# Kernel optimization log

Hardware: AMD Instinct MI355X
Metric: run time of the kernel (lower is better)

## Reference

```python
import jax, jax.numpy as jnp
import numpy as np

TOP_K = 8
N_GROUP = 8
TOPK_GROUP = 4
ROUTED_SCALING = 2.5
NORM_TOPK_PROB = True


def setup_inputs() -> dict:
    key = jax.random.key(0)
    k1, k2, k3 = jax.random.split(key, 3)
    bsz, seq_len, h = 4, 4096, 4096
    n_experts = 256
    hidden_states = jax.random.normal(k1, (bsz, seq_len, h), dtype=jnp.float32)
    # kaiming_uniform_(a=sqrt(5)) -> uniform(-1/sqrt(h), 1/sqrt(h)) approximately
    bound = 1.0 / np.sqrt(h)
    weight = jax.random.uniform(k2, (n_experts, h), dtype=jnp.float32, minval=-bound, maxval=bound)
    # correction bias is a buffer, zero-init; give it small random values to exercise the path
    e_score_correction_bias = jax.random.normal(k3, (n_experts,), dtype=jnp.float32) * 0.01
    return {"hidden_states": hidden_states, "weight": weight,
            "e_score_correction_bias": e_score_correction_bias}


def reference(hidden_states, weight, e_score_correction_bias):
    bsz, seq_len, h = hidden_states.shape
    n_experts = weight.shape[0]
    x = hidden_states.reshape(-1, h).astype(jnp.float32)          # [N, h]
    logits = jnp.einsum('nh,eh->ne', x, weight.astype(jnp.float32))  # [N, E]
    scores = jax.nn.sigmoid(logits)                                # [N, E]
    scores_for_choice = scores + e_score_correction_bias[None, :]  # [N, E]

    # group-limited routing: score each group by sum of its top-2 expert scores
    grouped = scores_for_choice.reshape(-1, N_GROUP, n_experts // N_GROUP)
    group_scores = jax.lax.top_k(grouped, 2)[0].sum(axis=-1)       # [N, G]
    _, group_idx = jax.lax.top_k(group_scores, TOPK_GROUP)         # [N, Kg]
    group_mask = jax.nn.one_hot(group_idx, N_GROUP, dtype=scores.dtype).sum(axis=1)  # [N, G]
    score_mask = jnp.repeat(group_mask, n_experts // N_GROUP, axis=-1)               # [N, E]

    tmp_scores = jnp.where(score_mask > 0, scores_for_choice, 0.0)
    _, topk_idx = jax.lax.top_k(tmp_scores, TOP_K)                 # [N, K]
    topk_weight = jnp.take_along_axis(scores, topk_idx, axis=1)    # [N, K] (no bias)

    if TOP_K > 1 and NORM_TOPK_PROB:
        denom = topk_weight.sum(axis=-1, keepdims=True) + 1e-20
        topk_weight = topk_weight / denom
    topk_weight = topk_weight * ROUTED_SCALING
    return topk_idx, topk_weight
```

## Files before the change

### kernel.cpp

```cpp
#include <hip/hip_runtime.h>
#include <math.h>

#define NTOK 16384
#define H 4096
#define NE 256
#define EPS_E 1.2e-5f
#define EPS_G 2.4e-5f
#define FIXCAP 1024
#define FLAGCAP 8192

typedef __attribute__((ext_vector_type(8))) short short8;
typedef __attribute__((ext_vector_type(4))) float f32x4;

__device__ __forceinline__ unsigned short f2bf(float x) {
    union { float f; unsigned u; } v; v.f = x;
    unsigned r = v.u + 0x7FFF + ((v.u >> 16) & 1);
    return (unsigned short)(r >> 16);
}
__device__ __forceinline__ float bf2f(unsigned short h) {
    union { float f; unsigned u; } v; v.u = ((unsigned)h) << 16;
    return v.f;
}

__global__ __launch_bounds__(256)
void split_w(const float* __restrict__ W, unsigned short* __restrict__ whi,
             unsigned short* __restrict__ wlo, int* __restrict__ ws)
{
    if (blockIdx.x == 0 && threadIdx.x == 0) ws[0] = 0;
    const int i = (blockIdx.x * 256 + threadIdx.x) * 4;
    float4 w4 = *(const float4*)(W + i);
    const float wv[4] = {w4.x, w4.y, w4.z, w4.w};
    ushort4 hh, ll;
    unsigned short* hp = (unsigned short*)&hh;
    unsigned short* lp = (unsigned short*)&ll;
    #pragma unroll
    for (int j = 0; j < 4; ++j) {
        unsigned short h = f2bf(wv[j]);
        hp[j] = h;
        lp[j] = f2bf(wv[j] - bf2f(h));
    }
    *(ushort4*)(whi + i) = hh;
    *(ushort4*)(wlo + i) = ll;
}

__global__ __launch_bounds__(256, 3)
void gemm3(const float* __restrict__ X, const unsigned short* __restrict__ Whi,
           const unsigned short* __restrict__ Wlo, float* __restrict__ logits,
           int m_base)
{
    __shared__ __align__(16) unsigned short smem[24576];
    unsigned short* Ah = smem;
    unsigned short* Al = smem + 4096;
    unsigned short* Bh = smem + 8192;
    unsigned short* Bl = smem + 16384;

    const int t = threadIdx.x;
    const int lane = t & 63;
    const int w = t >> 6;
    const int wm = w >> 1, wn = w & 1;
    const int fr = lane & 15, fq = lane >> 4;

    const int G = (int)gridDim.x;
    const int swz = (blockIdx.x & 7) * (G >> 3) + (blockIdx.x >> 3);
    const int nb = swz & 1;
    const int mb = swz >> 1;
    const int mloc = mb * 64;
    const int m0 = m_base + mloc;
    const int e0 = nb * 128;

    f32x4 acc[2][4];
    #pragma unroll
    for (int a = 0; a < 2; ++a)
        #pragma unroll
        for (int b = 0; b < 4; ++b) acc[a][b] = (f32x4){0.f, 0.f, 0.f, 0.f};

    const int ar = t >> 2;
    const int akc = t & 3;
    const float* gxa = X + (size_t)(m0 + ar) * H + akc * 16;

    const int blr = lane >> 3;
    const int bsrc = (lane & 7) ^ blr;
    const unsigned short* gbh = Whi + (size_t)(e0 + w * 8 + blr) * H + bsrc * 8;
    const unsigned short* gbl = Wlo + (size_t)(e0 + w * 8 + blr) * H + bsrc * 8;

    float4 xr0, xr1, xr2, xr3;
    auto loadX = [&](int kt) {
        const float* p = gxa + (size_t)kt * 64;
        xr0 = *(const float4*)p;       xr1 = *(const float4*)(p + 4);
        xr2 = *(const float4*)(p + 8); xr3 = *(const float4*)(p + 12);
    };

    loadX(0);

    #pragma unroll 1
    for (int kt = 0; kt < 64; ++kt) {
        __builtin_amdgcn_sched_barrier(0);
        __builtin_amdgcn_s_barrier();
        __builtin_amdgcn_sched_barrier(0);
        const size_t k0 = (size_t)kt * 64;
        #pragma unroll
        for (int i = 0; i < 4; ++i) {
            __builtin_amdgcn_global_load_lds(
                (const __attribute__((address_space(1))) void*)(gbh + (size_t)(32 * i) * H + k0),
                (__attribute__((address_space(3))) void*)&Bh[(w * 8 + 32 * i) * 64], 16, 0, 0);
            __builtin_amdgcn_global_load_lds(
                (const __attribute__((address_space(1))) void*)(gbl + (size_t)(32 * i) * H + k0),
                (__attribute__((address_space(3))) void*)&Bl[(w * 8 + 32 * i) * 64], 16, 0, 0);
        }
        __builtin_amdgcn_sched_barrier(0);
        asm volatile("s_waitcnt vmcnt(8)" ::: "memory");
        __builtin_amdgcn_sched_barrier(0);
        {
            const float xf[16] = {xr0.x, xr0.y, xr0.z, xr0.w, xr1.x, xr1.y, xr1.z, xr1.w,
                                  xr2.x, xr2.y, xr2.z, xr2.w, xr3.x, xr3.y, xr3.z, xr3.w};
            short8 h0, h1, l0, l1;
            #pragma unroll
            for (int j = 0; j < 16; ++j) {
                union { float f; unsigned u; } uu; uu.f = xf[j];
                union { unsigned u; float f; } hh; hh.u = uu.u & 0xFFFF0000u;
                union { float f; unsigned u; } ll; ll.f = xf[j] - hh.f;
                unsigned short hs = (unsigned short)(uu.u >> 16);
                unsigned short ls = (unsigned short)(ll.u >> 16);
                if (j < 8) { h0[j] = (short)hs; l0[j] = (short)ls; }
                else       { h1[j - 8] = (short)hs; l1[j - 8] = (short)ls; }
            }
            const int c0 = akc * 2;
            const int p0 = (c0 ^ (ar & 7)) * 8, p1 = ((c0 + 1) ^ (ar & 7)) * 8;
            *(short8*)&Ah[ar * 64 + p0] = h0;
            *(short8*)&Ah[ar * 64 + p1] = h1;
            *(short8*)&Al[ar * 64 + p0] = l0;
            *(short8*)&Al[ar * 64 + p1] = l1;
        }
        loadX(kt + 1 < 64 ? kt + 1 : 63);
        __builtin_amdgcn_sched_barrier(0);
        asm volatile("s_waitcnt vmcnt(4) lgkmcnt(0)" ::: "memory");
        __builtin_amdgcn_sched_barrier(0);
        __builtin_amdgcn_s_barrier();
        __builtin_amdgcn_sched_barrier(0);
        #pragma unroll
        for (int kk = 0; kk < 2; ++kk) {
            short8 ah[2], al[2], bh[4], bl[4];
            #pragma unroll
            for (int mt = 0; mt < 2; ++mt) {
                const int r = wm * 32 + mt * 16 + fr;
                const int pos = ((kk * 4 + fq) ^ (r & 7)) * 8;
                ah[mt] = *(const short8*)&Ah[r * 64 + pos];
                al[mt] = *(const short8*)&Al[r * 64 + pos];
            }
            #pragma unroll
            for (int nt = 0; nt < 4; ++nt) {
                const int r = wn * 64 + nt * 16 + fr;
                const int pos = ((kk * 4 + fq) ^ (r & 7)) * 8;
                bh[nt] = *(const short8*)&Bh[r * 64 + pos];
                bl[nt] = *(const short8*)&Bl[r * 64 + pos];
            }
            #pragma unroll
            for (int mt = 0; mt < 2; ++mt)
                #pragma unroll
                for (int nt = 0; nt < 4; ++nt)
                    acc[mt][nt] = __builtin_amdgcn_mfma_f32_16x16x32_bf16(ah[mt], bh[nt], acc[mt][nt], 0, 0, 0);
            #pragma unroll
            for (int mt = 0; mt < 2; ++mt)
                #pragma unroll
                for (int nt = 0; nt < 4; ++nt)
                    acc[mt][nt] = __builtin_amdgcn_mfma_f32_16x16x32_bf16(ah[mt], bl[nt], acc[mt][nt], 0, 0, 0);
            #pragma unroll
            for (int mt = 0; mt < 2; ++mt)
                #pragma unroll
                for (int nt = 0; nt < 4; ++nt)
                    acc[mt][nt] = __builtin_amdgcn_mfma_f32_16x16x32_bf16(al[mt], bh[nt], acc[mt][nt], 0, 0, 0);
        }
    }
    asm volatile("" :: "v"(xr0.x), "v"(xr1.x), "v"(xr2.x), "v"(xr3.x));

    #pragma unroll
    for (int mt = 0; mt < 2; ++mt)
        #pragma unroll
        for (int nt = 0; nt < 4; ++nt)
            #pragma unroll
            for (int r = 0; r < 4; ++r)
                logits[(size_t)(mloc + wm * 32 + mt * 16 + fq * 4 + r) * NE +
                       (e0 + wn * 64 + nt * 16 + fr)] = acc[mt][nt][r];
}

__global__ __launch_bounds__(256)
void route(const float* __restrict__ logits, const float* __restrict__ bias,
           float* __restrict__ out, int* __restrict__ ws, int cap, int m_base)
{
    const int t = threadIdx.x, lane = t & 63, wv = t >> 6;
    const float4 bf4 = *(const float4*)(bias + lane * 4);
    const float bfa[4] = {bf4.x, bf4.y, bf4.z, bf4.w};

    #pragma unroll 1
    for (int tt = 0; tt < 8; ++tt) {
        const int local = blockIdx.x * 32 + wv * 8 + tt;
        const int n = m_base + local;
        const float4 lg = *(const float4*)&logits[(size_t)local * NE + lane * 4];
        const float lga[4] = {lg.x, lg.y, lg.z, lg.w};
        float s[4], sc[4];
        #pragma unroll
        for (int i = 0; i < 4; ++i) {
            s[i] = 1.f / (1.f + expf(-lga[i]));
            sc[i] = s[i] + bfa[i];
        }
        float a1 = fmaxf(sc[0], sc[1]), a2 = fminf(sc[0], sc[1]);
        float b1 = fmaxf(sc[2], sc[3]), b2 = fminf(sc[2], sc[3]);
        float t1 = fmaxf(a1, b1);
        float t2 = fmaxf(fminf(a1, b1), fmaxf(a2, b2));
        #pragma unroll
        for (int off = 1; off <= 4; off <<= 1) {
            float o1 = __shfl_xor(t1, off, 64);
            float o2 = __shfl_xor(t2, off, 64);
            float n1 = fmaxf(t1, o1);
            float n2 = fmaxf(fminf(t1, o1), fmaxf(t2, o2));
            t1 = n1; t2 = n2;
        }
        const float gsum = t1 + t2;
        float gsv[8];
        #pragma unroll
        for (int g = 0; g < 8; ++g) gsv[g] = __shfl(gsum, g * 8, 64);

        float minsel = 3e38f, maxuns = -3e38f;
        bool sel = false;
        const int myg = lane >> 3;
        #pragma unroll
        for (int g = 0; g < 8; ++g) {
            int cg = 0;
            #pragma unroll
            for (int g2 = 0; g2 < 8; ++g2)
                cg += (gsv[g2] > gsv[g] || (gsv[g2] == gsv[g] && g2 < g)) ? 1 : 0;
            const bool sg = (cg < 4);
            if (sg) minsel = fminf(minsel, gsv[g]); else maxuns = fmaxf(maxuns, gsv[g]);
            if (myg == g) sel = sg;
        }
        bool flag = (minsel - maxuns) < EPS_G;

        float v[4];
        #pragma unroll
        for (int i = 0; i < 4; ++i) v[i] = sel ? sc[i] : 0.f;

        int idxs[8]; float sigs[8];
        float denom = 0.f, prevv = 0.f;
        #pragma unroll
        for (int r = 0; r < 9; ++r) {
            float bv = v[0]; int bi = 0; float bs = s[0];
            #pragma unroll
            for (int i = 1; i < 4; ++i)
                if (v[i] > bv) { bv = v[i]; bi = i; bs = s[i]; }
            int bidx = (lane << 2) + bi;
            #pragma unroll
            for (int off = 1; off < 64; off <<= 1) {
                float ov = __shfl_xor(bv, off, 64);
                int  oi = __shfl_xor(bidx, off, 64);
                float os = __shfl_xor(bs, off, 64);
                if (ov > bv || (ov == bv && oi < bidx)) { bv = ov; bidx = oi; bs = os; }
            }
            if (r > 0) flag = flag || ((prevv - bv) < EPS_E);
            prevv = bv;
            if (r < 8) {
                idxs[r] = bidx; sigs[r] = bs; denom += bs;
                if ((bidx >> 2) == lane) {
                    #pragma unroll
                    for (int i = 0; i < 4; ++i)
                        if ((bidx & 3) == i) v[i] = -3e38f;
                }
            }
        }
        denom += 1e-20f;
        #pragma unroll
        for (int r = 0; r < 8; ++r)
            if (lane == r) {
                out[n * 8 + r] = (float)idxs[r];
                out[NTOK * 8 + n * 8 + r] = sigs[r] / denom * 2.5f;
            }
        if (flag && lane == 0) {
            int slot = atomicAdd(ws, 1);
            if (slot < cap) ws[16 + slot] = n;
        }
    }
}

__global__ __launch_bounds__(256)
void fix1(const float* __restrict__ X, const float* __restrict__ W,
          const int* __restrict__ ws, double* __restrict__ fixlog, int cap)
{
    __shared__ float Xs4[4][4096];
    const int t = threadIdx.x, lane = t & 63, wv = t >> 6;
    int count = ws[0]; if (count > cap) count = cap;
    const int ngrp = (count + 3) >> 2;

    for (int task = blockIdx.x; task < ngrp * 8; task += (int)gridDim.x) {
        const int g = task >> 3, er = task & 7;
        int tok[4];
        #pragma unroll
        for (int q = 0; q < 4; ++q) {
            const int idx = g * 4 + q;
            tok[q] = ws[16 + (idx < count ? idx : g * 4)];
        }
        __syncthreads();
        #pragma unroll
        for (int q = 0; q < 4; ++q)
            for (int k = t * 4; k < 4096; k += 1024)
                *(float4*)&Xs4[q][k] = *(const float4*)(X + (size_t)tok[q] * H + k);
        __syncthreads();
        #pragma unroll 1
        for (int cc = 0; cc < 2; ++cc) {
            const int eb = er * 32 + wv * 8 + cc * 4;
            double a[4][4];
            #pragma unroll
            for (int q = 0; q < 4; ++q)
                #pragma unroll
                for (int ee = 0; ee < 4; ++ee) a[q][ee] = 0.0;
            for (int j = 0; j < 16; ++j) {
                const int kb = (lane + 64 * j) * 4;
                double xx[4][4];
                #pragma unroll
                for (int q = 0; q < 4; ++q) {
                    float4 x4 = *(const float4*)&Xs4[q][kb];
                    xx[q][0] = x4.x; xx[q][1] = x4.y; xx[q][2] = x4.z; xx[q][3] = x4.w;
                }
                #pragma unroll
                for (int ee = 0; ee < 4; ++ee) {
                    float4 w4 = *(const float4*)(W + (size_t)(eb + ee) * H + kb);
                    const double wd[4] = {w4.x, w4.y, w4.z, w4.w};
                    #pragma unroll
                    for (int q = 0; q < 4; ++q)
                        #pragma unroll
                        for (int kq = 0; kq < 4; ++kq)
                            a[q][ee] = fma(xx[q][kq], wd[kq], a[q][ee]);
                }
            }
            #pragma unroll
            for (int q = 0; q < 4; ++q)
                #pragma unroll
                for (int ee = 0; ee < 4; ++ee) {
                    double v = a[q][ee];
                    #pragma unroll
                    for (int off = 1; off < 64; off <<= 1)
                        v += __shfl_xor(v, off, 64);
                    if (lane == 0) fixlog[(size_t)(g * 4 + q) * NE + eb + ee] = v;
                }
        }
    }
}

__global__ __launch_bounds__(256)
void fix2(const double* __restrict__ fixlog, const float* __restrict__ bias,
          float* __restrict__ out, const int* __restrict__ ws, int cap)
{
    const int t = threadIdx.x, lane = t & 63, wv = t >> 6;
    int count = ws[0]; if (count > cap) count = cap;
    const int ngrp = (count + 3) >> 2;

    for (int g = blockIdx.x; g < ngrp; g += (int)gridDim.x) {
        const int idx = g * 4 + wv;
        const int slot = (idx < count) ? idx : g * 4;
        const int n = ws[16 + slot];
        const double* L = fixlog + (size_t)(g * 4 + wv) * NE;

        double s[4], sc[4];
        #pragma unroll
        for (int ii = 0; ii < 4; ++ii) {
            const double Lv = L[lane * 4 + ii];
            s[ii] = 1.0 / (1.0 + exp(-Lv));
            sc[ii] = s[ii] + (double)bias[lane * 4 + ii];
        }
        double a1 = fmax(sc[0], sc[1]), a2 = fmin(sc[0], sc[1]);
        double b1 = fmax(sc[2], sc[3]), b2 = fmin(sc[2], sc[3]);
        double t1 = fmax(a1, b1);
        double t2 = fmax(fmin(a1, b1), fmax(a2, b2));
        #pragma unroll
        for (int off = 1; off <= 4; off <<= 1) {
            double o1 = __shfl_xor(t1, off, 64);
            double o2 = __shfl_xor(t2, off, 64);
            double n1 = fmax(t1, o1);
            double n2 = fmax(fmin(t1, o1), fmax(t2, o2));
            t1 = n1; t2 = n2;
        }
        const double gsum = t1 + t2;
        double gsv[8];
        #pragma unroll
        for (int gg = 0; gg < 8; ++gg) gsv[gg] = __shfl(gsum, gg * 8, 64);
        const int myg = lane >> 3;
        int cnt = 0;
        #pragma unroll
        for (int gg = 0; gg < 8; ++gg)
            cnt += (gsv[gg] > gsum || (gsv[gg] == gsum && gg < myg)) ? 1 : 0;
        const bool sel = (cnt < 4);

        double v[4];
        #pragma unroll
        for (int ii = 0; ii < 4; ++ii) v[ii] = sel ? sc[ii] : 0.0;

        int idxs[8]; double sigs[8];
        double denom = 0.0;
        #pragma unroll
        for (int r = 0; r < 8; ++r) {
            double bv = v[0]; int bi = 0; double bs = s[0];
            #pragma unroll
            for (int ii = 1; ii < 4; ++ii)
                if (v[ii] > bv) { bv = v[ii]; bi = ii; bs = s[ii]; }
            int bidx = (lane << 2) + bi;
            #pragma unroll
            for (int off = 1; off < 64; off <<= 1) {
                double ov = __shfl_xor(bv, off, 64);
                int oi = __shfl_xor(bidx, off, 64);
                double os = __shfl_xor(bs, off, 64);
                if (ov > bv || (ov == bv && oi < bidx)) { bv = ov; bidx = oi; bs = os; }
            }
            idxs[r] = bidx; sigs[r] = bs; denom += bs;
            if ((bidx >> 2) == lane) {
                #pragma unroll
                for (int ii = 0; ii < 4; ++ii)
                    if ((bidx & 3) == ii) v[ii] = -1.0e300;
            }
        }
        denom += 1e-20;
        #pragma unroll
        for (int r = 0; r < 8; ++r)
            if (lane == r) {
                out[n * 8 + r] = (float)idxs[r];
                out[NTOK * 8 + n * 8 + r] = (float)(sigs[r] / denom * 2.5);
            }
    }
}

#define FXP 34
#define FEP 260
__global__ __launch_bounds__(256)
void moe_fb(const float* __restrict__ X, const float* __restrict__ W,
            const float* __restrict__ bias, float* __restrict__ out)
{
    __shared__ double Xs[16 * FXP];
    __shared__ double Ws[16 * FEP];
    const int t = threadIdx.x;
    const int lane = t & 63;
    const int wv = t >> 6;
    const int m0 = blockIdx.x * 32;
    double acc[8][4];
    #pragma unroll
    for (int i = 0; i < 8; ++i)
        #pragma unroll
        for (int j = 0; j < 4; ++j) acc[i][j] = 0.0;
    const int xm = t >> 3, xk = (t & 7) * 2;
    const int we = t >> 2, wk = (t & 3) * 4;
    const float* gx = X + (size_t)(m0 + xm) * H + xk;
    const float* gw = W + (size_t)we * H + wk;
    float2 xreg = *(const float2*)(gx);
    float4 wreg[4];
    #pragma unroll
    for (int p = 0; p < 4; ++p) wreg[p] = *(const float4*)(gw + (size_t)(64 * p) * H);
    const int NT = H / 16;
    for (int t0 = 0; t0 < NT; ++t0) {
        __syncthreads();
        Xs[(xk + 0) * FXP + xm] = (double)xreg.x;
        Xs[(xk + 1) * FXP + xm] = (double)xreg.y;
        #pragma unroll
        for (int p = 0; p < 4; ++p) {
            const int e = we + 64 * p;
            Ws[(wk + 0) * FEP + e] = (double)wreg[p].x;
            Ws[(wk + 1) * FEP + e] = (double)wreg[p].y;
            Ws[(wk + 2) * FEP + e] = (double)wreg[p].z;
            Ws[(wk + 3) * FEP + e] = (double)wreg[p].w;
        }
        __syncthreads();
        if (t0 + 1 < NT) {
            const int off = (t0 + 1) * 16;
            xreg = *(const float2*)(gx + off);
            #pragma unroll
            for (int p = 0; p < 4; ++p) wreg[p] = *(const float4*)(gw + (size_t)(64 * p) * H + off);
        }
        #pragma unroll
        for (int j = 0; j < 16; ++j) {
            const double* xrow = &Xs[j * FXP + wv * 8];
            const double2 wa = *(const double2*)&Ws[j * FEP + lane * 4];
            const double2 wb = *(const double2*)&Ws[j * FEP + lane * 4 + 2];
            const double ws4[4] = {wa.x, wa.y, wb.x, wb.y};
            #pragma unroll
            for (int mi = 0; mi < 8; ++mi)
                #pragma unroll
                for (int ei = 0; ei < 4; ++ei)
                    acc[mi][ei] = fma(xrow[mi], ws4[ei], acc[mi][ei]);
        }
    }
    const float4 bf = *(const float4*)(bias + lane * 4);
    const double bfa[4] = {(double)bf.x, (double)bf.y, (double)bf.z, (double)bf.w};
    #pragma unroll 1
    for (int tt = 0; tt < 8; ++tt) {
        double s[4], sc[4];
        #pragma unroll
        for (int i = 0; i < 4; ++i) {
            s[i] = 1.0 / (1.0 + exp(-acc[tt][i]));
            sc[i] = s[i] + bfa[i];
        }
        double a1 = fmax(sc[0], sc[1]), a2 = fmin(sc[0], sc[1]);
        double b1 = fmax(sc[2], sc[3]), b2 = fmin(sc[2], sc[3]);
        double t1 = fmax(a1, b1);
        double t2 = fmax(fmin(a1, b1), fmax(a2, b2));
        #pragma unroll
        for (int off = 1; off <= 4; off <<= 1) {
            double o1 = __shfl_xor(t1, off, 64);
            double o2 = __shfl_xor(t2, off, 64);
            double n1 = fmax(t1, o1);
            double n2 = fmax(fmin(t1, o1), fmax(t2, o2));
            t1 = n1; t2 = n2;
        }
        const double gsum = t1 + t2;
        double gsv[8];
        #pragma unroll
        for (int g = 0; g < 8; ++g) gsv[g] = __shfl(gsum, g * 8, 64);
        const int myg = lane >> 3;
        int cnt = 0;
        #pragma unroll
        for (int g = 0; g < 8; ++g)
            cnt += (gsv[g] > gsum || (gsv[g] == gsum && g < myg)) ? 1 : 0;
        const bool sel = (cnt < 4);
        double v[4];
        #pragma unroll
        for (int i = 0; i < 4; ++i) v[i] = sel ? sc[i] : 0.0;
        int idxs[8]; double sigs[8];
        double denom = 0.0;
        #pragma unroll
        for (int r = 0; r < 8; ++r) {
            double bv = v[0]; int bi = 0; double bs = s[0];
            #pragma unroll
            for (int i = 1; i < 4; ++i)
                if (v[i] > bv) { bv = v[i]; bi = i; bs = s[i]; }
            int bidx = (lane << 2) + bi;
            #pragma unroll
            for (int off = 1; off < 64; off <<= 1) {
                double ov = __shfl_xor(bv, off, 64);
                int oi = __shfl_xor(bidx, off, 64);
                double os = __shfl_xor(bs, off, 64);
                if (ov > bv || (ov == bv && oi < bidx)) { bv = ov; bidx = oi; bs = os; }
            }
            idxs[r] = bidx; sigs[r] = bs; denom += bs;
            if ((bidx >> 2) == lane) {
                #pragma unroll
                for (int i = 0; i < 4; ++i)
                    if ((bidx & 3) == i) v[i] = -1.0e300;
            }
        }
        denom += 1e-20;
        const size_t n = (size_t)(m0 + wv * 8 + tt);
        #pragma unroll
        for (int r = 0; r < 8; ++r)
            if (lane == r) {
                out[n * 8 + r] = (float)idxs[r];
                out[(size_t)NTOK * 8 + n * 8 + r] = (float)(sigs[r] / denom * 2.5);
            }
    }
}

extern "C" void kernel_launch(void* const* d_in, const int* in_sizes, int n_in,
                              void* d_out, int out_size, void* d_ws, size_t ws_size,
                              hipStream_t stream) {
    const float* X = (const float*)d_in[0];
    const float* W = (const float*)d_in[1];
    const float* bias = (const float*)d_in[2];
    float* out = (float*)d_out;

    const size_t WB = (size_t)NE * H * 2;
    const size_t OFF_W = 65536;
    const size_t OFF_FIX = OFF_W + 2 * WB;
    const size_t FIXB = (size_t)FIXCAP * NE * 8;
    const size_t OFF_LOG = OFF_FIX + FIXB;
    const size_t minlog = (size_t)256 * NE * 4;

    if (ws_size < OFF_LOG + minlog) {
        moe_fb<<<NTOK / 32, 256, 0, stream>>>(X, W, bias, out);
        return;
    }
    int* ws = (int*)d_ws;
    unsigned short* whi = (unsigned short*)((char*)d_ws + OFF_W);
    unsigned short* wlo = whi + (size_t)NE * H;
    double* fixlog = (double*)((char*)d_ws + OFF_FIX);
    float* logits = (float*)((char*)d_ws + OFF_LOG);

    split_w<<<(NE * H) / 1024, 256, 0, stream>>>(W, whi, wlo, ws);

    const size_t avail = ws_size - OFF_LOG;
    size_t full = (size_t)NTOK * NE * 4;
    int CT;
    if (avail >= full) CT = NTOK;
    else {
        CT = (int)(avail / ((size_t)NE * 4));
        CT &= ~255;
    }
    for (int mb0 = 0; mb0 < NTOK; mb0 += CT) {
        int ct = (NTOK - mb0 < CT) ? (NTOK - mb0) : CT;
        gemm3<<<(ct / 64) * 2, 256, 0, stream>>>(X, whi, wlo, logits, mb0);
        route<<<ct / 32, 256, 0, stream>>>(logits, bias, out, ws, FLAGCAP, mb0);
    }
    fix1<<<1024, 256, 0, stream>>>(X, W, ws, fixlog, FIXCAP);
    fix2<<<256, 256, 0, stream>>>(fixlog, bias, out, ws, FIXCAP);
}
```

Before: 221.9 us.

## Add split-K 128x128 GEMM path with two partial logit buffers

```diff
diff --git a/kernel.cpp b/kernel.cpp
--- a/kernel.cpp
+++ b/kernel.cpp
@@ -43,6 +43,252 @@
     *(ushort4*)(wlo + i) = ll;
 }
 
+__global__ __launch_bounds__(256, 2)
+void gemm3sk(const float* __restrict__ X, const unsigned short* __restrict__ Whi,
+             const unsigned short* __restrict__ Wlo,
+             float* __restrict__ logits0, float* __restrict__ logits1)
+{
+    __shared__ __align__(16) unsigned short smem[32768];
+    unsigned short* Ah = smem;
+    unsigned short* Al = smem + 8192;
+    unsigned short* Bh = smem + 16384;
+    unsigned short* Bl = smem + 24576;
+
+    const int t = threadIdx.x;
+    const int lane = t & 63;
+    const int w = t >> 6;
+    const int wm = w >> 1, wn = w & 1;
+    const int fr = lane & 15, fq = lane >> 4;
+
+    const int G = (int)gridDim.x;
+    const int swz = (blockIdx.x & 7) * (G >> 3) + (blockIdx.x >> 3);
+    const int kh = swz & 1;
+    const int nb = (swz >> 1) & 1;
+    const int mb = swz >> 2;
+    const int mloc = mb * 128;
+    const int e0 = nb * 128;
+    const int kbase = kh * 32;
+
+    f32x4 acc[4][4];
+    #pragma unroll
+    for (int a = 0; a < 4; ++a)
+        #pragma unroll
+        for (int b = 0; b < 4; ++b) acc[a][b] = (f32x4){0.f, 0.f, 0.f, 0.f};
+
+    const int ar = t >> 1;
+    const int ah2 = t & 1;
+    const float* gxa = X + (size_t)(mloc + ar) * H + ah2 * 32;
+
+    const int blr = lane >> 3;
+    const int bsrc = (lane & 7) ^ blr;
+    const unsigned short* gbh = Whi + (size_t)(e0 + w * 8 + blr) * H + bsrc * 8;
+    const unsigned short* gbl = Wlo + (size_t)(e0 + w * 8 + blr) * H + bsrc * 8;
+
+    float4 xr0, xr1, xr2, xr3, xr4, xr5, xr6, xr7;
+    auto loadX = [&](int kt) {
+        const float* p = gxa + (size_t)kt * 64;
+        xr0 = *(const float4*)p;        xr1 = *(const float4*)(p + 4);
+        xr2 = *(const float4*)(p + 8);  xr3 = *(const float4*)(p + 12);
+        xr4 = *(const float4*)(p + 16); xr5 = *(const float4*)(p + 20);
+        xr6 = *(const float4*)(p + 24); xr7 = *(const float4*)(p + 28);
+    };
+
+    loadX(kbase);
+
+    #pragma unroll 1
+    for (int ks = 0; ks < 32; ++ks) {
+        const int kt = kbase + ks;
+        __builtin_amdgcn_sched_barrier(0);
+        __builtin_amdgcn_s_barrier();
+        __builtin_amdgcn_sched_barrier(0);
+        const size_t k0 = (size_t)kt * 64;
+        #pragma unroll
+        for (int i = 0; i < 4; ++i) {
+            __builtin_amdgcn_global_load_lds(
+                (const __attribute__((address_space(1))) void*)(gbh + (size_t)(32 * i) * H + k0),
+                (__attribute__((address_space(3))) void*)&Bh[(w * 8 + 32 * i) * 64], 16, 0, 0);
+            __builtin_amdgcn_global_load_lds(
+                (const __attribute__((address_space(1))) void*)(gbl + (size_t)(32 * i) * H + k0),
+                (__attribute__((address_space(3))) void*)&Bl[(w * 8 + 32 * i) * 64], 16, 0, 0);
+        }
+        __builtin_amdgcn_sched_barrier(0);
+        asm volatile("s_waitcnt vmcnt(8)" ::: "memory");
+        __builtin_amdgcn_sched_barrier(0);
+        {
+            const float xf[32] = {xr0.x, xr0.y, xr0.z, xr0.w, xr1.x, xr1.y, xr1.z, xr1.w,
+                                  xr2.x, xr2.y, xr2.z, xr2.w, xr3.x, xr3.y, xr3.z, xr3.w,
+                                  xr4.x, xr4.y, xr4.z, xr4.w, xr5.x, xr5.y, xr5.z, xr5.w,
+                                  xr6.x, xr6.y, xr6.z, xr6.w, xr7.x, xr7.y, xr7.z, xr7.w};
+            #pragma unroll
+            for (int c = 0; c < 4; ++c) {
+                short8 h8, l8;
+                #pragma unroll
+                for (int j = 0; j < 8; ++j) {
+                    union { float f; unsigned u; } uu; uu.f = xf[c * 8 + j];
+                    union { unsigned u; float f; } hh; hh.u = uu.u & 0xFFFF0000u;
+                    union { float f; unsigned u; } ll; ll.f = xf[c * 8 + j] - hh.f;
+                    h8[j] = (short)(uu.u >> 16);
+                    l8[j] = (short)(ll.u >> 16);
+                }
+                const int cc = ah2 * 4 + c;
+                const int pos = (cc ^ (ar & 7)) * 8;
+                *(short8*)&Ah[ar * 64 + pos] = h8;
+                *(short8*)&Al[ar * 64 + pos] = l8;
+            }
+        }
+        loadX(ks + 1 < 32 ? kt + 1 : kt);
+        __builtin_amdgcn_sched_barrier(0);
+        asm volatile("s_waitcnt vmcnt(8) lgkmcnt(0)" ::: "memory");
+        __builtin_amdgcn_sched_barrier(0);
+        __builtin_amdgcn_s_barrier();
+        __builtin_amdgcn_sched_barrier(0);
+        #pragma unroll
+        for (int kk = 0; kk < 2; ++kk) {
+            short8 ah[4], al[4], bh[4], bl[4];
+            #pragma unroll
+            for (int mt = 0; mt < 4; ++mt) {
+                const int r = wm * 64 + mt * 16 + fr;
+                const int pos = ((kk * 4 + fq) ^ (r & 7)) * 8;
+                ah[mt] = *(const short8*)&Ah[r * 64 + pos];
+                al[mt] = *(const short8*)&Al[r * 64 + pos];
+            }
+            #pragma unroll
+            for (int nt = 0; nt < 4; ++nt) {
+                const int r = wn * 64 + nt * 16 + fr;
+                const int pos = ((kk * 4 + fq) ^ (r & 7)) * 8;
+                bh[nt] = *(const short8*)&Bh[r * 64 + pos];
+                bl[nt] = *(const short8*)&Bl[r * 64 + pos];
+            }
+            #pragma unroll
+            for (int mt = 0; mt < 4; ++mt)
+                #pragma unroll
+                for (int nt = 0; nt < 4; ++nt)
+                    acc[mt][nt] = __builtin_amdgcn_mfma_f32_16x16x32_bf16(ah[mt], bh[nt], acc[mt][nt], 0, 0, 0);
+            #pragma unroll
+            for (int mt = 0; mt < 4; ++mt)
+                #pragma unroll
+                for (int nt = 0; nt < 4; ++nt)
+                    acc[mt][nt] = __builtin_amdgcn_mfma_f32_16x16x32_bf16(ah[mt], bl[nt], acc[mt][nt], 0, 0, 0);
+            #pragma unroll
+            for (int mt = 0; mt < 4; ++mt)
+                #pragma unroll
+                for (int nt = 0; nt < 4; ++nt)
+                    acc[mt][nt] = __builtin_amdgcn_mfma_f32_16x16x32_bf16(al[mt], bh[nt], acc[mt][nt], 0, 0, 0);
+        }
+    }
+    asm volatile("" :: "v"(xr0.x), "v"(xr1.x), "v"(xr2.x), "v"(xr3.x),
+                       "v"(xr4.x), "v"(xr5.x), "v"(xr6.x), "v"(xr7.x));
+    asm volatile("s_waitcnt vmcnt(0) lgkmcnt(0)" ::: "memory");
+
+    float* lgout = kh ? logits1 : logits0;
+    #pragma unroll
+    for (int mt = 0; mt < 4; ++mt)
+        #pragma unroll
+        for (int nt = 0; nt < 4; ++nt)
+            #pragma unroll
+            for (int r = 0; r < 4; ++r)
+                lgout[(size_t)(mloc + wm * 64 + mt * 16 + fq * 4 + r) * NE +
+                      (e0 + wn * 64 + nt * 16 + fr)] = acc[mt][nt][r];
+}
+
+__global__ __launch_bounds__(256)
+void route2(const float* __restrict__ l0, const float* __restrict__ l1,
+            const float* __restrict__ bias, float* __restrict__ out,
+            int* __restrict__ ws, int cap)
+{
+    const int t = threadIdx.x, lane = t & 63, wv = t >> 6;
+    const float4 bf4 = *(const float4*)(bias + lane * 4);
+    const float bfa[4] = {bf4.x, bf4.y, bf4.z, bf4.w};
+
+    #pragma unroll 1
+    for (int tt = 0; tt < 8; ++tt) {
+        const int n = blockIdx.x * 32 + wv * 8 + tt;
+        const float4 ga = *(const float4*)&l0[(size_t)n * NE + lane * 4];
+        const float4 gb = *(const float4*)&l1[(size_t)n * NE + lane * 4];
+        const float lga[4] = {ga.x + gb.x, ga.y + gb.y, ga.z + gb.z, ga.w + gb.w};
+        float s[4], sc[4];
+        #pragma unroll
+        for (int i = 0; i < 4; ++i) {
+            s[i] = 1.f / (1.f + expf(-lga[i]));
+            sc[i] = s[i] + bfa[i];
+        }
+        float a1 = fmaxf(sc[0], sc[1]), a2 = fminf(sc[0], sc[1]);
+        float b1 = fmaxf(sc[2], sc[3]), b2 = fminf(sc[2], sc[3]);
+        float t1 = fmaxf(a1, b1);
+        float t2 = fmaxf(fminf(a1, b1), fmaxf(a2, b2));
+        #pragma unroll
+        for (int off = 1; off <= 4; off <<= 1) {
+            float o1 = __shfl_xor(t1, off, 64);
+            float o2 = __shfl_xor(t2, off, 64);
+            float n1 = fmaxf(t1, o1);
+            float n2 = fmaxf(fminf(t1, o1), fmaxf(t2, o2));
+            t1 = n1; t2 = n2;
+        }
+        const float gsum = t1 + t2;
+        float gsv[8];
+        #pragma unroll
+        for (int g = 0; g < 8; ++g) gsv[g] = __shfl(gsum, g * 8, 64);
+
+        float minsel = 3e38f, maxuns = -3e38f;
+        bool sel = false;
+        const int myg = lane >> 3;
+        #pragma unroll
+        for (int g = 0; g < 8; ++g) {
+            int cg = 0;
+            #pragma unroll
+            for (int g2 = 0; g2 < 8; ++g2)
+                cg += (gsv[g2] > gsv[g] || (gsv[g2] == gsv[g] && g2 < g)) ? 1 : 0;
+            const bool sg = (cg < 4);
+            if (sg) minsel = fminf(minsel, gsv[g]); else maxuns = fmaxf(maxuns, gsv[g]);
+            if (myg == g) sel = sg;
+        }
+        bool flag = (minsel - maxuns) < EPS_G;
+
+        float v[4];
+        #pragma unroll
+        for (int i = 0; i < 4; ++i) v[i] = sel ? sc[i] : 0.f;
+
+        int idxs[8]; float sigs[8];
+        float denom = 0.f, prevv = 0.f;
+        #pragma unroll
+        for (int r = 0; r < 9; ++r) {
+            float bv = v[0]; int bi = 0; float bs = s[0];
+            #pragma unroll
+            for (int i = 1; i < 4; ++i)
+                if (v[i] > bv) { bv = v[i]; bi = i; bs = s[i]; }
+            int bidx = (lane << 2) + bi;
+            #pragma unroll
+            for (int off = 1; off < 64; off <<= 1) {
+                float ov = __shfl_xor(bv, off, 64);
+                int  oi = __shfl_xor(bidx, off, 64);
+                float os = __shfl_xor(bs, off, 64);
+                if (ov > bv || (ov == bv && oi < bidx)) { bv = ov; bidx = oi; bs = os; }
+            }
+            if (r > 0) flag = flag || ((prevv - bv) < EPS_E);
+            prevv = bv;
+            if (r < 8) {
+                idxs[r] = bidx; sigs[r] = bs; denom += bs;
+                if ((bidx >> 2) == lane) {
+                    #pragma unroll
+                    for (int i = 0; i < 4; ++i)
+                        if ((bidx & 3) == i) v[i] = -3e38f;
+                }
+            }
+        }
+        denom += 1e-20f;
+        #pragma unroll
+        for (int r = 0; r < 8; ++r)
+            if (lane == r) {
+                out[n * 8 + r] = (float)idxs[r];
+                out[NTOK * 8 + n * 8 + r] = sigs[r] / denom * 2.5f;
+            }
+        if (flag && lane == 0) {
+            int slot = atomicAdd(ws, 1);
+            if (slot < cap) ws[16 + slot] = n;
+        }
+    }
+}
+
 __global__ __launch_bounds__(256, 3)
 void gemm3(const float* __restrict__ X, const unsigned short* __restrict__ Whi,
            const unsigned short* __restrict__ Wlo, float* __restrict__ logits,
@@ -566,6 +812,7 @@
     const size_t FIXB = (size_t)FIXCAP * NE * 8;
     const size_t OFF_LOG = OFF_FIX + FIXB;
     const size_t minlog = (size_t)256 * NE * 4;
+    const size_t full = (size_t)NTOK * NE * 4;
 
     if (ws_size < OFF_LOG + minlog) {
         moe_fb<<<NTOK / 32, 256, 0, stream>>>(X, W, bias, out);
@@ -576,21 +823,27 @@
     unsigned short* wlo = whi + (size_t)NE * H;
     double* fixlog = (double*)((char*)d_ws + OFF_FIX);
     float* logits = (float*)((char*)d_ws + OFF_LOG);
+    const size_t avail = ws_size - OFF_LOG;
 
     split_w<<<(NE * H) / 1024, 256, 0, stream>>>(W, whi, wlo, ws);
 
-    const size_t avail = ws_size - OFF_LOG;
-    size_t full = (size_t)NTOK * NE * 4;
-    int CT;
-    if (avail >= full) CT = NTOK;
-    else {
-        CT = (int)(avail / ((size_t)NE * 4));
-        CT &= ~255;
-    }
-    for (int mb0 = 0; mb0 < NTOK; mb0 += CT) {
-        int ct = (NTOK - mb0 < CT) ? (NTOK - mb0) : CT;
-        gemm3<<<(ct / 64) * 2, 256, 0, stream>>>(X, whi, wlo, logits, mb0);
-        route<<<ct / 32, 256, 0, stream>>>(logits, bias, out, ws, FLAGCAP, mb0);
+    if (avail >= 2 * full) {
+        float* l0 = logits;
+        float* l1 = logits + (size_t)NTOK * NE;
+        gemm3sk<<<512, 256, 0, stream>>>(X, whi, wlo, l0, l1);
+        route2<<<NTOK / 32, 256, 0, stream>>>(l0, l1, bias, out, ws, FLAGCAP);
+    } else {
+        int CT;
+        if (avail >= full) CT = NTOK;
+        else {
+            CT = (int)(avail / ((size_t)NE * 4));
+            CT &= ~255;
+        }
+        for (int mb0 = 0; mb0 < NTOK; mb0 += CT) {
+            int ct = (NTOK - mb0 < CT) ? (NTOK - mb0) : CT;
+            gemm3<<<(ct / 64) * 2, 256, 0, stream>>>(X, whi, wlo, logits, mb0);
+            route<<<ct / 32, 256, 0, stream>>>(logits, bias, out, ws, FLAGCAP, mb0);
+        }
     }
     fix1<<<1024, 256, 0, stream>>>(X, W, ws, fixlog, FIXCAP);
     fix2<<<256, 256, 0, stream>>>(fixlog, bias, out, ws, FIXCAP);
```

New measurement: 228.6 us. +3.0%, slower.
